# Performance work log

Measured on AMD Instinct MI355X. Metric: run time of the kernel, lower is better.

The kernel has to match this reference:

```python
import jax, jax.numpy as jnp
import numpy as np

# --- config (mirrors args) ---
ANCHORS = np.array([(10,13),(16,30),(33,23),(30,61),(62,45),(59,119),
                    (116,90),(156,198),(373,326)], dtype=np.float32)
IMG = 512.0
NUM_CLASSES = 80
NUM_LOCAL = 3           # num_anchors_per_resolution
IOU_THR = 0.5
LAMBDA_COORD, LAMBDA_OBJ, LAMBDA_NOOBJ, LAMBDA_CLS = 5.0, 1.0, 0.5, 1.0
EPS = 1e-12


def setup_inputs() -> dict:
    key = jax.random.key(0)
    k1, k2, k3, k4 = jax.random.split(key, 4)
    B, T, G = 16, 50, 64
    backbone_out = jax.random.normal(k1, (B, NUM_LOCAL * (5 + NUM_CLASSES), G, G), dtype=jnp.float32)
    xy = jax.random.uniform(k2, (B, T, 2), minval=0.02, maxval=0.98)
    wh = jax.random.uniform(k3, (B, T, 2), minval=0.10, maxval=0.90)
    cls = jax.random.randint(k4, (B, T, 1), 0, NUM_CLASSES).astype(jnp.float32)
    gt_targets = jnp.concatenate([xy, wh, cls], axis=-1)  # [B,T,5] = x,y,w,h,cls
    return {"backbone_out": backbone_out, "gt_targets": gt_targets}


def _bce(p, y):
    p = jnp.clip(p, EPS, 1.0 - EPS)
    return -(y * jnp.log(p) + (1.0 - y) * jnp.log(1.0 - p))


def _get_target(gt, anchors_grid, a0, in_h, in_w):
    """Vectorized version of get_target. gt: [B,T,5]. anchors_grid: [9,2] in grid units.
    Out-of-range rows are routed to an out-of-bounds scatter index, which JAX drops."""
    B, T, _ = gt.shape
    valid = gt.sum(-1) > 0                                   # [B,T]
    gx = gt[..., 0] * in_w
    gy = gt[..., 1] * in_h
    gw = gt[..., 2] * in_w
    gh = gt[..., 3] * in_h
    gi = gy.astype(jnp.int32)                                # int() truncation (gy>=0)
    gj = gx.astype(jnp.int32)
    cls_idx = gt[..., 4].astype(jnp.int32)

    aw, ah = anchors_grid[:, 0], anchors_grid[:, 1]
    # IoU of (0,0,gw,gh) vs (0,0,aw,ah) corner boxes
    inter = jnp.minimum(gw[..., None], aw) * jnp.minimum(gh[..., None], ah)
    union = gw[..., None] * gh[..., None] + aw * ah - inter
    ious = inter / (union + 1e-16)                           # [B,T,9]

    b_idx = jnp.broadcast_to(jnp.arange(B)[:, None], (B, T))

    # ---- noobj mask: zero the cell for every local anchor with IoU > thr ----
    local_ious = ious[..., a0:a0 + NUM_LOCAL]                # [B,T,3]
    cond_no = valid[..., None] & (local_ious > IOU_THR)
    gi3 = jnp.where(cond_no, gi[..., None], in_h)            # OOB => dropped
    gj3 = jnp.broadcast_to(gj[..., None], (B, T, NUM_LOCAL))
    b3 = jnp.broadcast_to(b_idx[..., None], (B, T, NUM_LOCAL))
    a3 = jnp.broadcast_to(jnp.arange(NUM_LOCAL), (B, T, NUM_LOCAL))
    noobj = jnp.ones((B, NUM_LOCAL, in_h, in_w), jnp.float32)
    noobj = noobj.at[b3, a3, gi3, gj3].min(jnp.zeros((B, T, NUM_LOCAL), jnp.float32))

    # ---- positive assignment: global-best anchor, kept only if in this scale's triple ----
    best = jnp.argmax(ious, axis=-1)                          # [B,T] global anchor id
    local = best - a0
    hit = valid & (local >= 0) & (local < NUM_LOCAL)
    gi_s = jnp.where(hit, gi, in_h)                           # OOB => dropped
    local_c = jnp.clip(local, 0, NUM_LOCAL - 1)

    tx_v = gx - gj.astype(jnp.float32)
    ty_v = gy - gi.astype(jnp.float32)
    tw_v = jnp.log(gw / aw[best] + 1e-16)
    th_v = jnp.log(gh / ah[best] + 1e-16)

    zeros = jnp.zeros((B, NUM_LOCAL, in_h, in_w), jnp.float32)
    ones_bt = jnp.ones((B, T), jnp.float32)
    mask = zeros.at[b_idx, local_c, gi_s, gj].max(ones_bt)
    t_x = zeros.at[b_idx, local_c, gi_s, gj].set(tx_v)
    t_y = zeros.at[b_idx, local_c, gi_s, gj].set(ty_v)
    t_w = zeros.at[b_idx, local_c, gi_s, gj].set(tw_v)
    t_h = zeros.at[b_idx, local_c, gi_s, gj].set(th_v)
    t_conf = mask
    t_cls = jnp.zeros((B, NUM_LOCAL, in_h, in_w, NUM_CLASSES), jnp.float32)
    t_cls = t_cls.at[b_idx, local_c, gi_s, gj, cls_idx].max(ones_bt)
    return mask, noobj, t_x, t_y, t_w, t_h, t_conf, t_cls


def reference(backbone_out, gt_targets):
    B, _, in_w, in_h = backbone_out.shape   # source names shape[2]=in_w, shape[3]=in_h (square)
    scale_w = IMG / in_w
    a0 = {32.0: 0, 16.0: 3, 8.0: 6}[scale_w]
    anchors_grid = jnp.asarray(ANCHORS / scale_w)
    attr = 5 + NUM_CLASSES

    preds = backbone_out.reshape(B, NUM_LOCAL, attr, in_h, in_w).transpose(0, 1, 3, 4, 2)
    t_x = jax.nn.sigmoid(preds[..., 0])
    t_y = jax.nn.sigmoid(preds[..., 1])
    t_w = preds[..., 2]
    t_h = preds[..., 3]
    pred_conf = jax.nn.sigmoid(preds[..., 4])
    pred_cls = jax.nn.sigmoid(preds[..., 5:])

    gt = jax.lax.stop_gradient(gt_targets)   # targets are constants (requires_grad=False)
    mask, noobj, x0, y0, w, h, gt_conf, gt_cls = _get_target(gt, anchors_grid, a0, in_h, in_w)

    n_obj = jnp.maximum(mask.sum(), 1.0)
    n_noobj = jnp.maximum(noobj.sum(), 1.0)

    # masked MSE == MSELoss over boolean-selected elements
    loss_x = (mask * (t_x - x0) ** 2).sum() / n_obj
    loss_y = (mask * (t_y - y0) ** 2).sum() / n_obj
    loss_w = (mask * (t_w - w) ** 2).sum() / n_obj
    loss_h = (mask * (t_h - h) ** 2).sum() / n_obj

    bce_conf = _bce(pred_conf, gt_conf)
    loss_obj = (mask * bce_conf).sum() / n_obj
    loss_noobj = (noobj * bce_conf).sum() / n_noobj

    # cls_count is None => uniform weights of 1 => plain masked mean over obj*num_classes elems
    loss_cls = (mask[..., None] * _bce(pred_cls, gt_cls)).sum() / (n_obj * NUM_CLASSES)

    bbox_loss = LAMBDA_COORD * (loss_x + loss_y + loss_w + loss_h)
    objectness_loss = LAMBDA_OBJ * loss_obj + LAMBDA_NOOBJ * loss_noobj
    cls_loss = LAMBDA_CLS * loss_cls
    loss_total = bbox_loss + objectness_loss + cls_loss
    return loss_total, bbox_loss, objectness_loss, cls_loss
```

## Files before the change

### kernel.cpp

```cpp
#include <hip/hip_runtime.h>
#include <math.h>

#define BB 16
#define TT 50
#define GG 64
#define NLOC 3
#define NCLS 80
#define NATTR 85
#define NCH 255
#define NCELLS (BB*NLOC*GG*GG)
#define NB_DENSE (NCELLS/256)
#define NB_TGT (BB*TT)
#define NB_TOTAL (NB_DENSE + NB_TGT)
#define NP 12
#define CLAMP_BCE 27.631021f

__constant__ float c_AW[9] = {1.25f, 2.0f, 4.125f, 3.75f, 7.75f, 7.375f, 14.5f, 19.5f, 46.625f};
__constant__ float c_AH[9] = {1.625f, 3.75f, 2.875f, 7.625f, 5.625f, 14.875f, 11.25f, 24.75f, 40.75f};

struct TG {
    int   valid, hit, gi, gj, local, cls, best;
    float gx, gy, gw, gh, il0, il1, il2;
};

__device__ __forceinline__ float softplus_c(float z) {
    float sp = fmaxf(z, 0.f) + log1pf(expf(-fabsf(z)));
    return fminf(sp, CLAMP_BCE);
}
__device__ __forceinline__ float sigmoidf_(float z) { return 1.f / (1.f + expf(-z)); }

__device__ __forceinline__ TG compute_tgt(const float* __restrict__ gt, int b, int i) {
    TG r;
    const float* g = gt + (b * TT + i) * 5;
    float x = g[0], y = g[1], w = g[2], h = g[3], c = g[4];
    r.valid = (x + y + w + h + c) > 0.f;
    r.gx = x * 64.f; r.gy = y * 64.f; r.gw = w * 64.f; r.gh = h * 64.f;
    r.gi = (int)r.gy;
    r.gj = (int)r.gx;
    r.cls = (int)c;
    float bi = -1.f; int ba = 0;
    float il[3] = {0.f, 0.f, 0.f};
    #pragma unroll
    for (int a = 0; a < 9; a++) {
        float aw = c_AW[a], ah = c_AH[a];
        float inter = fminf(r.gw, aw) * fminf(r.gh, ah);
        float uni   = r.gw * r.gh + aw * ah - inter;
        float iou   = inter / (uni + 1e-16f);
        if (iou > bi) { bi = iou; ba = a; }
        if (a >= 6) il[a - 6] = iou;
    }
    r.best = ba; r.il0 = il[0]; r.il1 = il[1]; r.il2 = il[2];
    r.local = ba - 6;
    r.hit = r.valid && (r.local >= 0) && (r.local < NLOC);
    return r;
}

__global__ void __launch_bounds__(256) k_main(const float* __restrict__ bb,
                                              const float* __restrict__ gt,
                                              float* __restrict__ partial) {
    int blk = blockIdx.x;
    int tid = threadIdx.x;

    if (blk < NB_DENSE) {
        __shared__ float s;
        if (tid == 0) s = 0.f;
        __syncthreads();
        int idx   = blk * 256 + tid;
        int plane = idx >> 12, off = idx & 4095;
        int b = plane / 3, a = plane - b * 3;
        float v = softplus_c(bb[((b * NCH + a * NATTR + 4) << 12) + off]);
        #pragma unroll
        for (int o = 32; o > 0; o >>= 1) v += __shfl_down(v, o);
        if ((tid & 63) == 0) atomicAdd(&s, v);
        __syncthreads();
        if (tid < NP) partial[blk * NP + tid] = (tid == 0) ? s : 0.f;
        return;
    }

    __shared__ TG tg[TT];
    __shared__ float acc[NP];
    __shared__ unsigned clsmask[3];
    __shared__ int notwin, zeroed;
    int t = blk - NB_DENSE;
    int b = t / TT, i = t - b * TT;

    if (tid < NP) acc[tid] = 0.f;
    if (tid < 3) clsmask[tid] = 0u;
    if (tid == 0) { notwin = 0; zeroed = 0; }
    if (tid < TT) tg[tid] = compute_tgt(gt, b, tid);
    __syncthreads();

    TG R = tg[i];
    int cell = R.hit ? (((b * NLOC + R.local) * GG + R.gi) * GG + R.gj) : -1;

    if (R.hit && tid < TT) {
        TG q = tg[tid];
        int cj = q.hit ? (((b * NLOC + q.local) * GG + q.gi) * GG + q.gj) : -1;
        if (cj == cell) {
            if (tid > i) notwin = 1;
            atomicOr(&clsmask[q.cls >> 5], 1u << (q.cls & 31));
        }
        float ilr = (R.local == 0) ? q.il0 : (R.local == 1) ? q.il1 : q.il2;
        if (q.valid && q.gi == R.gi && q.gj == R.gj && ilr > 0.5f) zeroed = 1;
    }
    __syncthreads();

    if (R.hit && !notwin) {
        int base = ((b * NCH + R.local * NATTR) << 12) + (R.gi << 6) + R.gj;
        if (tid < NCLS) {
            unsigned y = (clsmask[tid >> 5] >> (tid & 31)) & 1u;
            float z = bb[base + ((5 + tid) << 12)];
            atomicAdd(&acc[6], y ? softplus_c(-z) : softplus_c(z));
        } else if (tid < NCLS + 5) {
            int attr = tid - NCLS;
            float z = bb[base + (attr << 12)];
            if (attr == 0)      { float tx = R.gx - (float)R.gj; float d = sigmoidf_(z) - tx; acc[1] = d * d; }
            else if (attr == 1) { float ty = R.gy - (float)R.gi; float d = sigmoidf_(z) - ty; acc[2] = d * d; }
            else if (attr == 2) { float tw = logf(R.gw / c_AW[R.best] + 1e-16f); float d = z - tw; acc[3] = d * d; }
            else if (attr == 3) { float th = logf(R.gh / c_AH[R.best] + 1e-16f); float d = z - th; acc[4] = d * d; }
            else {
                float b1 = softplus_c(-z);
                acc[5] = b1;
                if (!zeroed) acc[7] = b1 - softplus_c(z);
                acc[8] = 1.f;
            }
        }
    }
    __syncthreads();
    if (tid < NP) partial[blk * NP + tid] = acc[tid];
}

__global__ void __launch_bounds__(256) k_final(const float* __restrict__ bb,
                                               const float* __restrict__ gt,
                                               const float* __restrict__ partial,
                                               float* __restrict__ out) {
    __shared__ unsigned bitmap[NCELLS / 32];
    __shared__ float red[NP];
    __shared__ float s_sub;
    __shared__ int s_nz;
    int tid = threadIdx.x;

    for (int i = tid; i < NCELLS / 32; i += 256) bitmap[i] = 0u;
    if (tid < NP) red[tid] = 0.f;
    if (tid == 0) { s_sub = 0.f; s_nz = 0; }
    __syncthreads();

    float s[9];
    #pragma unroll
    for (int c = 0; c < 9; c++) s[c] = 0.f;
    for (int idx = tid; idx < NB_TOTAL; idx += 256) {
        const float* p = partial + idx * NP;
        #pragma unroll
        for (int c = 0; c < 9; c++) s[c] += p[c];
    }
    #pragma unroll
    for (int c = 0; c < 9; c++) {
        float v = s[c];
        #pragma unroll
        for (int o = 32; o > 0; o >>= 1) v += __shfl_down(v, o);
        if ((tid & 63) == 0) atomicAdd(&red[c], v);
    }

    for (int t = tid; t < BB * TT; t += 256) {
        int b = t / TT, i = t - b * TT;
        TG r = compute_tgt(gt, b, i);
        if (r.valid) {
            float il[3] = {r.il0, r.il1, r.il2};
            #pragma unroll
            for (int a = 0; a < NLOC; a++) {
                if (il[a] > 0.5f) {
                    int cell = ((b * NLOC + a) * GG + r.gi) * GG + r.gj;
                    atomicOr(&bitmap[cell >> 5], 1u << (cell & 31));
                }
            }
        }
    }
    __syncthreads();

    int nz = 0; float sub = 0.f;
    for (int wI = tid; wI < NCELLS / 32; wI += 256) {
        unsigned u = bitmap[wI];
        nz += __popc(u);
        while (u) {
            int bit = __ffs(u) - 1;
            u &= u - 1;
            int cell  = wI * 32 + bit;
            int plane = cell >> 12, off = cell & 4095;
            int b = plane / 3, a = plane - b * 3;
            sub += softplus_c(bb[((b * NCH + a * NATTR + 4) << 12) + off]);
        }
    }
    {
        float v = sub;
        int n = nz;
        #pragma unroll
        for (int o = 32; o > 0; o >>= 1) { v += __shfl_down(v, o); n += __shfl_down(n, o); }
        if ((tid & 63) == 0) { atomicAdd(&s_sub, v); atomicAdd(&s_nz, n); }
    }
    __syncthreads();

    if (tid == 0) {
        float nobj = fmaxf(red[8], 1.f);
        float nno  = fmaxf((float)NCELLS - (float)s_nz, 1.f);
        float bbox = 5.f * (red[1] + red[2] + red[3] + red[4]) / nobj;
        float objl = red[5] / nobj + 0.5f * (red[0] - s_sub + red[7]) / nno;
        float clsl = red[6] / (nobj * (float)NCLS);
        out[0] = bbox + objl + clsl;
        out[1] = bbox;
        out[2] = objl;
        out[3] = clsl;
    }
}

extern "C" void kernel_launch(void* const* d_in, const int* in_sizes, int n_in,
                              void* d_out, int out_size, void* d_ws, size_t ws_size,
                              hipStream_t stream) {
    const float* bb = (const float*)d_in[0];
    const float* gt = (const float*)d_in[1];
    float* partial = (float*)d_ws;
    float* out = (float*)d_out;

    k_main <<<NB_TOTAL, 256, 0, stream>>>(bb, gt, partial);
    k_final<<<1,        256, 0, stream>>>(bb, gt, partial, out);
}
```

Measured before the change: 118.3 us.

## Move noobj-cell correction into per-target blocks and vectorize dense conf pass

The single-block final kernel no longer builds a shared bitmap of every noobj-zeroed cell and then scans it serially. Instead, each target block handles its own three local anchors. It credits a zeroed cell only if no earlier target in the same image claims the same cell, and accumulates that cell's softplus and a count into new partial slots. The dense confidence pass now reads float4 values in 128-thread blocks (192 blocks in total), and the final kernel only reduces 11 partial columns. The risk is a small serial ownership loop per target, plus a correct-deduplication requirement that replaces the bitmap's implicit uniqueness.

```diff
diff --git a/kernel.cpp b/kernel.cpp
--- a/kernel.cpp
+++ b/kernel.cpp
@@ -9,7 +9,7 @@
 #define NATTR 85
 #define NCH 255
 #define NCELLS (BB*NLOC*GG*GG)
-#define NB_DENSE (NCELLS/256)
+#define NB_DENSE 192
 #define NB_TGT (BB*TT)
 #define NB_TOTAL (NB_DENSE + NB_TGT)
 #define NP 12
@@ -55,25 +55,30 @@
     return r;
 }
 
-__global__ void __launch_bounds__(256) k_main(const float* __restrict__ bb,
+__global__ void __launch_bounds__(128) k_main(const float* __restrict__ bb,
                                               const float* __restrict__ gt,
                                               float* __restrict__ partial) {
     int blk = blockIdx.x;
     int tid = threadIdx.x;
 
     if (blk < NB_DENSE) {
-        __shared__ float s;
-        if (tid == 0) s = 0.f;
+        const float4* bb4 = (const float4*)bb;
+        float v = 0.f;
+        #pragma unroll
+        for (int r = 0; r < 2; r++) {
+            int idx4  = blk * 256 + r * 128 + tid;
+            int plane = idx4 >> 10;
+            int off4  = idx4 & 1023;
+            int b = plane / 3, a = plane - b * 3;
+            float4 q = bb4[((b * NCH + a * NATTR + 4) << 10) + off4];
+            v += softplus_c(q.x) + softplus_c(q.y) + softplus_c(q.z) + softplus_c(q.w);
+        }
+        #pragma unroll
+        for (int o = 32; o > 0; o >>= 1) v += __shfl_down(v, o);
+        __shared__ float sred[2];
+        if ((tid & 63) == 0) sred[tid >> 6] = v;
         __syncthreads();
-        int idx   = blk * 256 + tid;
-        int plane = idx >> 12, off = idx & 4095;
-        int b = plane / 3, a = plane - b * 3;
-        float v = softplus_c(bb[((b * NCH + a * NATTR + 4) << 12) + off]);
-        #pragma unroll
-        for (int o = 32; o > 0; o >>= 1) v += __shfl_down(v, o);
-        if ((tid & 63) == 0) atomicAdd(&s, v);
-        __syncthreads();
-        if (tid < NP) partial[blk * NP + tid] = (tid == 0) ? s : 0.f;
+        if (tid < NP) partial[blk * NP + tid] = (tid == 0) ? (sred[0] + sred[1]) : 0.f;
         return;
     }
 
@@ -91,11 +96,28 @@
     __syncthreads();
 
     TG R = tg[i];
-    int cell = R.hit ? (((b * NLOC + R.local) * GG + R.gi) * GG + R.gj) : -1;
-
+
+    if (tid < 3 && R.valid) {
+        float ila = (tid == 0) ? R.il0 : (tid == 1) ? R.il1 : R.il2;
+        if (ila > 0.5f) {
+            bool own = true;
+            for (int j = 0; j < i; j++) {
+                TG q = tg[j];
+                float ilq = (tid == 0) ? q.il0 : (tid == 1) ? q.il1 : q.il2;
+                if (q.valid && q.gi == R.gi && q.gj == R.gj && ilq > 0.5f) { own = false; break; }
+            }
+            if (own) {
+                float z = bb[((b * NCH + tid * NATTR + 4) << 12) + (R.gi << 6) + R.gj];
+                atomicAdd(&acc[9], softplus_c(z));
+                atomicAdd(&acc[10], 1.f);
+            }
+        }
+    }
+
+    int cell = R.hit ? ((R.local << 12) + (R.gi << 6) + R.gj) : -1;
     if (R.hit && tid < TT) {
         TG q = tg[tid];
-        int cj = q.hit ? (((b * NLOC + q.local) * GG + q.gi) * GG + q.gj) : -1;
+        int cj = q.hit ? ((q.local << 12) + (q.gi << 6) + q.gj) : -1;
         if (cj == cell) {
             if (tid > i) notwin = 1;
             atomicOr(&clsmask[q.cls >> 5], 1u << (q.cls & 31));
@@ -130,80 +152,35 @@
     if (tid < NP) partial[blk * NP + tid] = acc[tid];
 }
 
-__global__ void __launch_bounds__(256) k_final(const float* __restrict__ bb,
-                                               const float* __restrict__ gt,
-                                               const float* __restrict__ partial,
+__global__ void __launch_bounds__(256) k_final(const float* __restrict__ partial,
                                                float* __restrict__ out) {
-    __shared__ unsigned bitmap[NCELLS / 32];
     __shared__ float red[NP];
-    __shared__ float s_sub;
-    __shared__ int s_nz;
     int tid = threadIdx.x;
-
-    for (int i = tid; i < NCELLS / 32; i += 256) bitmap[i] = 0u;
     if (tid < NP) red[tid] = 0.f;
-    if (tid == 0) { s_sub = 0.f; s_nz = 0; }
-    __syncthreads();
-
-    float s[9];
+    __syncthreads();
+
+    float s[11];
     #pragma unroll
-    for (int c = 0; c < 9; c++) s[c] = 0.f;
+    for (int c = 0; c < 11; c++) s[c] = 0.f;
     for (int idx = tid; idx < NB_TOTAL; idx += 256) {
         const float* p = partial + idx * NP;
         #pragma unroll
-        for (int c = 0; c < 9; c++) s[c] += p[c];
+        for (int c = 0; c < 11; c++) s[c] += p[c];
     }
     #pragma unroll
-    for (int c = 0; c < 9; c++) {
+    for (int c = 0; c < 11; c++) {
         float v = s[c];
         #pragma unroll
         for (int o = 32; o > 0; o >>= 1) v += __shfl_down(v, o);
         if ((tid & 63) == 0) atomicAdd(&red[c], v);
     }
-
-    for (int t = tid; t < BB * TT; t += 256) {
-        int b = t / TT, i = t - b * TT;
-        TG r = compute_tgt(gt, b, i);
-        if (r.valid) {
-            float il[3] = {r.il0, r.il1, r.il2};
-            #pragma unroll
-            for (int a = 0; a < NLOC; a++) {
-                if (il[a] > 0.5f) {
-                    int cell = ((b * NLOC + a) * GG + r.gi) * GG + r.gj;
-                    atomicOr(&bitmap[cell >> 5], 1u << (cell & 31));
-                }
-            }
-        }
-    }
-    __syncthreads();
-
-    int nz = 0; float sub = 0.f;
-    for (int wI = tid; wI < NCELLS / 32; wI += 256) {
-        unsigned u = bitmap[wI];
-        nz += __popc(u);
-        while (u) {
-            int bit = __ffs(u) - 1;
-            u &= u - 1;
-            int cell  = wI * 32 + bit;
-            int plane = cell >> 12, off = cell & 4095;
-            int b = plane / 3, a = plane - b * 3;
-            sub += softplus_c(bb[((b * NCH + a * NATTR + 4) << 12) + off]);
-        }
-    }
-    {
-        float v = sub;
-        int n = nz;
-        #pragma unroll
-        for (int o = 32; o > 0; o >>= 1) { v += __shfl_down(v, o); n += __shfl_down(n, o); }
-        if ((tid & 63) == 0) { atomicAdd(&s_sub, v); atomicAdd(&s_nz, n); }
-    }
     __syncthreads();
 
     if (tid == 0) {
         float nobj = fmaxf(red[8], 1.f);
-        float nno  = fmaxf((float)NCELLS - (float)s_nz, 1.f);
+        float nno  = fmaxf((float)NCELLS - red[10], 1.f);
         float bbox = 5.f * (red[1] + red[2] + red[3] + red[4]) / nobj;
-        float objl = red[5] / nobj + 0.5f * (red[0] - s_sub + red[7]) / nno;
+        float objl = red[5] / nobj + 0.5f * (red[0] - red[9] + red[7]) / nno;
         float clsl = red[6] / (nobj * (float)NCLS);
         out[0] = bbox + objl + clsl;
         out[1] = bbox;
@@ -220,6 +197,6 @@
     float* partial = (float*)d_ws;
     float* out = (float*)d_out;
 
-    k_main <<<NB_TOTAL, 256, 0, stream>>>(bb, gt, partial);
-    k_final<<<1,        256, 0, stream>>>(bb, gt, partial, out);
-}
+    k_main <<<NB_TOTAL, 128, 0, stream>>>(bb, gt, partial);
+    k_final<<<1,        256, 0, stream>>>(partial, out);
+}
```

After: 103.1 us. -12.8%, faster.
